# Performance work log

Measured on AMD Instinct MI355X. Metric: run time of the kernel, lower is better.

## Reference

```python
import jax, jax.numpy as jnp
import numpy as np
from math import log, sqrt

B, S, D, H, L = 16, 512, 512, 8, 6
DPH = D // H
DFF = 2048
VOCAB = 1024
MAXDEG = 64
NPC, NS = 4096, 4096


def setup_inputs() -> dict:
    rng = np.random.default_rng(0)
    raw_x = rng.integers(0, VOCAB + 1, (B, S)).astype(np.int32)
    scatter_degree = rng.integers(0, MAXDEG + 1, (B, S)).astype(np.int32)

    def uniq_triples(n, seed):
        r = np.random.default_rng(seed)
        flat = r.choice(B * S * S, n, replace=False)  # unique (b,i,j)
        b, i, j = np.unravel_index(flat, (B, S, S))
        return np.stack([b, i, j], 1).astype(np.int32)

    parentchild_indices = uniq_triples(NPC, 1)
    silbing_indices = uniq_triples(NS, 2)
    parent_child_now = np.stack([np.arange(B), rng.integers(0, S, B)], 1).astype(np.int32)
    silbing_now = np.stack([np.arange(B), rng.integers(0, S, B)], 1).astype(np.int32)

    key = jax.random.key(0)
    ks = jax.random.split(key, 16)
    sc = 0.02
    inp = {
        "raw_x": jnp.asarray(raw_x),
        "scatter_degree": jnp.asarray(scatter_degree),
        "parentchild_indices": jnp.asarray(parentchild_indices),
        "parent_child_now": jnp.asarray(parent_child_now),
        "silbing_indices": jnp.asarray(silbing_indices),
        "silbing_now": jnp.asarray(silbing_now),
        "vocab_emb": jax.random.normal(ks[0], (VOCAB + 1, D), jnp.float32) * sc,
        "degree_emb": jax.random.normal(ks[1], (MAXDEG + 1, D), jnp.float32) * sc,
        "active_rel_emb": jax.random.normal(ks[2], (2, D), jnp.float32) * sc,
        "relation_encoder": jax.random.uniform(ks[3], (3,), jnp.float32),
        "Wq": jax.random.normal(ks[4], (L, D, D), jnp.float32) * sc,
        "bq": jnp.zeros((L, D), jnp.float32),
        "Wk": jax.random.normal(ks[5], (L, D, D), jnp.float32) * sc,
        "bk": jnp.zeros((L, D), jnp.float32),
        "Wv": jax.random.normal(ks[6], (L, D, D), jnp.float32) * sc,
        "bv": jnp.zeros((L, D), jnp.float32),
        "Wo": jax.random.normal(ks[7], (L, D, D), jnp.float32) * sc,
        "bo": jnp.zeros((L, D), jnp.float32),
        "W1": jax.random.normal(ks[8], (L, DFF, D), jnp.float32) * sc,
        "b1": jnp.zeros((L, DFF), jnp.float32),
        "W2": jax.random.normal(ks[9], (L, D, DFF), jnp.float32) * sc,
        "b2": jnp.zeros((L, D), jnp.float32),
        "ln_g": jnp.ones((L, D), jnp.float32),
        "ln_b": jnp.zeros((L, D), jnp.float32),
        "logits_w": jax.random.normal(ks[10], (VOCAB, D), jnp.float32) * sc,
    }
    return inp


def _layer_norm(x, g, b):
    m = jnp.mean(x, -1, keepdims=True)
    v = jnp.mean((x - m) ** 2, -1, keepdims=True)  # biased var, eps=1e-5 (torch default)
    return (x - m) * jax.lax.rsqrt(v + 1e-5) * g + b


def _forward(raw_x, scatter_degree, parentchild_indices, parent_child_now,
             silbing_indices, silbing_now, vocab_emb, degree_emb, active_rel_emb,
             relation_encoder, Wq, bq, Wk, bk, Wv, bv, Wo, bo, W1, b1, W2, b2,
             ln_g, ln_b, logits_w):
    x = vocab_emb[raw_x]  # [B,S,D]
    # sinusoidal positional encoding
    pos = jnp.arange(S, dtype=jnp.float32)[:, None]
    div = jnp.exp(jnp.arange(0, D, 2, dtype=jnp.float32) * (-log(10000.0) / D))
    pe = jnp.zeros((S, D), x.dtype).at[:, 0::2].set(jnp.sin(pos * div)).at[:, 1::2].set(jnp.cos(pos * div))
    x = x + pe
    # structural encodings
    x = x + degree_emb[scatter_degree]
    x = x.at[parent_child_now[:, 0], parent_child_now[:, 1]].add(active_rel_emb[0])
    x = x.at[silbing_now[:, 0], silbing_now[:, 1]].add(active_rel_emb[1])

    pb, pi, pj = parentchild_indices[:, 0], parentchild_indices[:, 1], parentchild_indices[:, 2]
    sb, si, sj = silbing_indices[:, 0], silbing_indices[:, 1], silbing_indices[:, 2]
    inv_norm = 1.0 / sqrt(DPH)

    for l in range(L):
        q = (x @ Wq[l].T + bq[l]).reshape(B, S, H, DPH).transpose(0, 2, 1, 3)
        k = (x @ Wk[l].T + bk[l]).reshape(B, S, H, DPH).transpose(0, 2, 1, 3)
        v = (x @ Wv[l].T + bv[l]).reshape(B, S, H, DPH).transpose(0, 2, 1, 3)
        scores = jnp.einsum('bhqd,bhkd->bhqk', q, k) * inv_norm  # [B,H,S,S]
        # scatter-added relational bias (broadcast over all heads)
        scores = scores.at[pb, :, pi, pj].add(relation_encoder[0])
        scores = scores.at[pb, :, pj, pi].add(relation_encoder[1])
        scores = scores.at[sb, :, si, sj].add(relation_encoder[2])
        scores = scores.at[sb, :, sj, si].add(relation_encoder[2])
        attn = jax.nn.softmax(scores, axis=-1)
        o = jnp.einsum('bhqk,bhkd->bhqd', attn, v).transpose(0, 2, 1, 3).reshape(B, S, D)
        o = o @ Wo[l].T + bo[l]
        x = _layer_norm(x + o, ln_g[l], ln_b[l])
        ff = jax.nn.relu(x @ W1[l].T + b1[l]) @ W2[l].T + b2[l]
        x = _layer_norm(x + ff, ln_g[l], ln_b[l])

    return x[:, -1] @ logits_w.T  # [B, VOCAB]


def reference(raw_x, scatter_degree, parentchild_indices, parent_child_now,
              silbing_indices, silbing_now, vocab_emb, degree_emb, active_rel_emb,
              relation_encoder, Wq, bq, Wk, bk, Wv, bv, Wo, bo, W1, b1, W2, b2,
              ln_g, ln_b, logits_w):
    return _forward(raw_x, scatter_degree, parentchild_indices, parent_child_now,
                    silbing_indices, silbing_now, vocab_emb, degree_emb, active_rel_emb,
                    relation_encoder, Wq, bq, Wk, bk, Wv, bv, Wo, bo, W1, b1, W2, b2,
                    ln_g, ln_b, logits_w)
```

## Files before the change

### kernel.cpp

```cpp
#include <hip/hip_runtime.h>
#include <hip/hip_bf16.h>
#include <math.h>

#define B_ 16
#define S_ 512
#define D_ 512
#define H_ 8
#define L_ 6
#define DPH_ 64
#define DFF_ 2048
#define VOCAB_ 1024
#define NPC_ 4096
#define NS_ 4096
#define BS_ (B_ * S_)
#define LOG2E 1.4426950408889634f

typedef __attribute__((ext_vector_type(8))) short bf16x8;
typedef __attribute__((ext_vector_type(4))) float f32x4;

__device__ __forceinline__ ushort f2bf(float f) {
    __hip_bfloat16 h = __float2bfloat16(f);
    return __builtin_bit_cast(ushort, h);
}
__device__ __forceinline__ float bf2f(ushort u) {
    unsigned int v = ((unsigned int)u) << 16;
    return __builtin_bit_cast(float, v);
}

__global__ __launch_bounds__(256) void embed_kernel(
    const int* __restrict__ raw_x, const int* __restrict__ sdeg,
    const float* __restrict__ vemb, const float* __restrict__ demb,
    float* __restrict__ x)
{
    size_t idx = (size_t)blockIdx.x * 256 + threadIdx.x;
    int d = (int)(idx & (D_ - 1));
    size_t bs = idx >> 9;
    int s = (int)(bs & (S_ - 1));
    int tok = raw_x[bs];
    int dg  = sdeg[bs];
    float e = expf(-(float)(d & ~1) * (9.210340371976184f / (float)D_));
    float ang = (float)s * e;
    float pe = (d & 1) ? cosf(ang) : sinf(ang);
    x[idx] = vemb[(size_t)tok * D_ + d] + pe + demb[(size_t)dg * D_ + d];
}

__global__ void relnow_kernel(const int* __restrict__ pcn, const int* __restrict__ sbn,
                              const float* __restrict__ arel, float* __restrict__ x)
{
    int b = blockIdx.x;
    int t = threadIdx.x;
    int b1 = pcn[b * 2 + 0], p1 = pcn[b * 2 + 1];
    x[((size_t)(b1 * S_ + p1)) * D_ + t] += arel[t];
    int b2 = sbn[b * 2 + 0], p2 = sbn[b * 2 + 1];
    x[((size_t)(b2 * S_ + p2)) * D_ + t] += arel[D_ + t];
}

__global__ void bias_scatter_kernel(const int* __restrict__ pc, const int* __restrict__ sb,
                                    const float* __restrict__ renc, float* __restrict__ bias)
{
    int t = blockIdx.x * 256 + threadIdx.x;
    float r0 = renc[0], r1 = renc[1], r2 = renc[2];
    if (t < NPC_) {
        int b = pc[t * 3 + 0], i = pc[t * 3 + 1], j = pc[t * 3 + 2];
        atomicAdd(&bias[((size_t)b * S_ + i) * S_ + j], r0);
        atomicAdd(&bias[((size_t)b * S_ + j) * S_ + i], r1);
    } else if (t < NPC_ + NS_) {
        int u = t - NPC_;
        int b = sb[u * 3 + 0], i = sb[u * 3 + 1], j = sb[u * 3 + 2];
        atomicAdd(&bias[((size_t)b * S_ + i) * S_ + j], r2);
        atomicAdd(&bias[((size_t)b * S_ + j) * S_ + i], r2);
    }
}

__global__ __launch_bounds__(256) void bias_cast_kernel(const float* __restrict__ src,
                                                        ushort* __restrict__ dst)
{
    int i = blockIdx.x * 256 + threadIdx.x;
    float4 v = ((const float4*)src)[i];
    ushort4 o;
    o.x = f2bf(v.x * LOG2E); o.y = f2bf(v.y * LOG2E);
    o.z = f2bf(v.z * LOG2E); o.w = f2bf(v.w * LOG2E);
    ((ushort4*)dst)[i] = o;
}

__global__ __launch_bounds__(256) void cast4_kernel(const float* __restrict__ src,
                                                    ushort* __restrict__ dst, int n4)
{
    int i = blockIdx.x * 256 + threadIdx.x;
    if (i >= n4) return;
    float4 v = ((const float4*)src)[i];
    ushort4 o;
    o.x = f2bf(v.x); o.y = f2bf(v.y); o.z = f2bf(v.z); o.w = f2bf(v.w);
    ((ushort4*)dst)[i] = o;
}

__global__ __launch_bounds__(256) void pack_qkv_kernel(
    const float* __restrict__ Wq, const float* __restrict__ Wk, const float* __restrict__ Wv,
    ushort* __restrict__ dst)
{
    int idx = blockIdx.x * 256 + threadIdx.x;
    int c = idx & 511;
    int rl = idx >> 9;
    int r = rl % 1536, l = rl / 1536;
    float v;
    if (r < 512)       v = Wq[((size_t)l * 512 + r) * 512 + c];
    else if (r < 1024) v = Wk[((size_t)l * 512 + (r - 512)) * 512 + c];
    else               v = Wv[((size_t)l * 512 + (r - 1024)) * 512 + c];
    dst[idx] = f2bf(v);
}

__global__ void pack_bqkv_kernel(const float* __restrict__ bq, const float* __restrict__ bk,
                                 const float* __restrict__ bv, float* __restrict__ dst)
{
    int idx = blockIdx.x * 256 + threadIdx.x;
    if (idx >= L_ * 1536) return;
    int r = idx % 1536, l = idx / 1536;
    float v;
    if (r < 512)       v = bq[l * 512 + r];
    else if (r < 1024) v = bk[l * 512 + r - 512];
    else               v = bv[l * 512 + r - 1024];
    dst[idx] = v;
}

#define GL2LDS(g, l) __builtin_amdgcn_global_load_lds( \
    (const __attribute__((address_space(1))) void*)(g), \
    (__attribute__((address_space(3))) void*)(l), 16, 0, 0)

__global__ __launch_bounds__(256) void gemm_bf16(
    const ushort* __restrict__ A, const ushort* __restrict__ W,
    const float* __restrict__ bias, ushort* __restrict__ Cb,
    int K, int M, int mode)
{
    __shared__ ushort As[128 * 32];
    __shared__ ushort Bs[128 * 32];

    const int t  = threadIdx.x;
    const int wv = t >> 6;
    const int ln = t & 63;
    const int wm = wv >> 1, wn = wv & 1;
    const int row0 = blockIdx.y * 128;
    const int col0 = blockIdx.x * 128;
    const int lr = ln >> 2;
    const int lk = (ln & 3) * 8;

    f32x4 acc[4][4] = {};

    for (int k0 = 0; k0 < K; k0 += 32) {
        #pragma unroll
        for (int i = 0; i < 2; i++) {
            int r = i * 64 + wv * 16;
            const ushort* ga = A + (size_t)(row0 + r + lr) * K + k0 + lk;
            const ushort* gb = W + (size_t)(col0 + r + lr) * K + k0 + lk;
            GL2LDS(ga, &As[r * 32]);
            GL2LDS(gb, &Bs[r * 32]);
        }
        __syncthreads();

        bf16x8 af[4], bf[4];
        #pragma unroll
        for (int mi = 0; mi < 4; mi++)
            af[mi] = *(const bf16x8*)&As[(wm * 64 + mi * 16 + (ln & 15)) * 32 + (ln >> 4) * 8];
        #pragma unroll
        for (int ni = 0; ni < 4; ni++)
            bf[ni] = *(const bf16x8*)&Bs[(wn * 64 + ni * 16 + (ln & 15)) * 32 + (ln >> 4) * 8];
        #pragma unroll
        for (int mi = 0; mi < 4; mi++)
            #pragma unroll
            for (int ni = 0; ni < 4; ni++)
                acc[mi][ni] = __builtin_amdgcn_mfma_f32_16x16x32_bf16(af[mi], bf[ni], acc[mi][ni], 0, 0, 0);
        __syncthreads();
    }

    const int lq = ln >> 4, lc = ln & 15;
    #pragma unroll
    for (int mi = 0; mi < 4; mi++) {
        #pragma unroll
        for (int ni = 0; ni < 4; ni++) {
            int gcol = col0 + wn * 64 + ni * 16 + lc;
            float bb = bias[gcol];
            #pragma unroll
            for (int rr = 0; rr < 4; rr++) {
                int grow = row0 + wm * 64 + mi * 16 + lq * 4 + rr;
                float val = acc[mi][ni][rr] + bb;
                if (mode == 1) val = fmaxf(val, 0.f);
                Cb[(size_t)grow * M + gcol] = f2bf(val);
            }
        }
    }
}

__global__ __launch_bounds__(256) void gemm_bf16_sk(
    const ushort* __restrict__ A, const ushort* __restrict__ W,
    ushort* __restrict__ Cp, int K, int M)
{
    __shared__ ushort As[128 * 32];
    __shared__ ushort Bs[128 * 32];

    const int t  = threadIdx.x;
    const int wv = t >> 6;
    const int ln = t & 63;
    const int wm = wv >> 1, wn = wv & 1;
    const int row0 = blockIdx.y * 128;
    const int col0 = blockIdx.x * 128;
    const int z    = blockIdx.z;
    const int Kh   = K >> 1;
    const int lr = ln >> 2;
    const int lk = (ln & 3) * 8;

    const ushort* Az = A + (size_t)z * Kh;
    const ushort* Wz = W + (size_t)z * Kh;

    f32x4 acc[4][4] = {};

    for (int k0 = 0; k0 < Kh; k0 += 32) {
        #pragma unroll
        for (int i = 0; i < 2; i++) {
            int r = i * 64 + wv * 16;
            const ushort* ga = Az + (size_t)(row0 + r + lr) * K + k0 + lk;
            const ushort* gb = Wz + (size_t)(col0 + r + lr) * K + k0 + lk;
            GL2LDS(ga, &As[r * 32]);
            GL2LDS(gb, &Bs[r * 32]);
        }
        __syncthreads();

        bf16x8 af[4], bf[4];
        #pragma unroll
        for (int mi = 0; mi < 4; mi++)
            af[mi] = *(const bf16x8*)&As[(wm * 64 + mi * 16 + (ln & 15)) * 32 + (ln >> 4) * 8];
        #pragma unroll
        for (int ni = 0; ni < 4; ni++)
            bf[ni] = *(const bf16x8*)&Bs[(wn * 64 + ni * 16 + (ln & 15)) * 32 + (ln >> 4) * 8];
        #pragma unroll
        for (int mi = 0; mi < 4; mi++)
            #pragma unroll
            for (int ni = 0; ni < 4; ni++)
                acc[mi][ni] = __builtin_amdgcn_mfma_f32_16x16x32_bf16(af[mi], bf[ni], acc[mi][ni], 0, 0, 0);
        __syncthreads();
    }

    ushort* Cz = Cp + (size_t)z * BS_ * M;
    const int lq = ln >> 4, lc = ln & 15;
    #pragma unroll
    for (int mi = 0; mi < 4; mi++)
        #pragma unroll
        for (int ni = 0; ni < 4; ni++) {
            int gcol = col0 + wn * 64 + ni * 16 + lc;
            #pragma unroll
            for (int rr = 0; rr < 4; rr++) {
                int grow = row0 + wm * 64 + mi * 16 + lq * 4 + rr;
                Cz[(size_t)grow * M + gcol] = f2bf(acc[mi][ni][rr]);
            }
        }
}

#define PSTR 72

__device__ __forceinline__ int vswz(int d, int j) {
    int g = ((j >> 3) ^ (d & 7) ^ ((d >> 3) & 7)) & 7;
    return d * 64 + g * 8 + (j & 7);
}

__global__ __launch_bounds__(256) void attn_kernel(
    const ushort* __restrict__ qkv, const ushort* __restrict__ biasb,
    ushort* __restrict__ ao)
{
    const int qt = blockIdx.x, h = blockIdx.y, b = blockIdx.z;
    const int t  = threadIdx.x;
    const int wq = t >> 6;
    const int ln = t & 63;
    const int lq = ln >> 4;
    const int lc = ln & 15;
    const int r  = t >> 2;
    const int cg = t & 3;

    __shared__ ushort Qs[64 * PSTR];
    __shared__ ushort Ks[64 * PSTR];
    __shared__ ushort Ps[64 * PSTR];
    __shared__ ushort Vts[64 * 64];

    const int i0 = qt * 64;

    {
        const ushort* qsrc = qkv + (size_t)(b * S_ + i0 + r) * 1536 + h * 64 + cg * 16;
        *(uint4*)&Qs[r * PSTR + cg * 16]     = ((const uint4*)qsrc)[0];
        *(uint4*)&Qs[r * PSTR + cg * 16 + 8] = ((const uint4*)qsrc)[1];
    }
    bf16x8 aq0 = *(const bf16x8*)&Qs[(wq * 16 + lc) * PSTR + lq * 8];
    bf16x8 aq1 = *(const bf16x8*)&Qs[(wq * 16 + lc) * PSTR + 32 + lq * 8];

    f32x4 of[4] = {};
    float l_lane[4] = {};
    const float QSC = 0.125f * LOG2E;

    for (int j0 = 0; j0 < S_; j0 += 64) {
        __syncthreads();
        {
            const ushort* ksrc = qkv + (size_t)(b * S_ + j0 + r) * 1536 + 512 + h * 64 + cg * 16;
            *(uint4*)&Ks[r * PSTR + cg * 16]     = ((const uint4*)ksrc)[0];
            *(uint4*)&Ks[r * PSTR + cg * 16 + 8] = ((const uint4*)ksrc)[1];
            const ushort* vsrc = ksrc + 512;
            ushort vv[16];
            *(uint4*)&vv[0] = ((const uint4*)vsrc)[0];
            *(uint4*)&vv[8] = ((const uint4*)vsrc)[1];
            #pragma unroll
            for (int dd = 0; dd < 16; dd++)
                Vts[vswz(cg * 16 + dd, r)] = vv[dd];
        }
        __syncthreads();

        f32x4 sf[4] = {};
        #pragma unroll
        for (int ni = 0; ni < 4; ni++) {
            bf16x8 bk0 = *(const bf16x8*)&Ks[(ni * 16 + lc) * PSTR + lq * 8];
            bf16x8 bk1 = *(const bf16x8*)&Ks[(ni * 16 + lc) * PSTR + 32 + lq * 8];
            sf[ni] = __builtin_amdgcn_mfma_f32_16x16x32_bf16(aq0, bk0, sf[ni], 0, 0, 0);
            sf[ni] = __builtin_amdgcn_mfma_f32_16x16x32_bf16(aq1, bk1, sf[ni], 0, 0, 0);
        }

        const ushort* bbase = biasb + (size_t)(b * S_ + i0 + wq * 16 + lq * 4) * S_ + j0;
        #pragma unroll
        for (int ni = 0; ni < 4; ni++)
            #pragma unroll
            for (int rr = 0; rr < 4; rr++) {
                float bv = bf2f(bbase[(size_t)rr * S_ + ni * 16 + lc]);
                float p = __builtin_amdgcn_exp2f(fmaf(sf[ni][rr], QSC, bv));
                l_lane[rr] += p;
                Ps[(wq * 16 + lq * 4 + rr) * PSTR + ni * 16 + lc] = f2bf(p);
            }

        bf16x8 ap0 = *(const bf16x8*)&Ps[(wq * 16 + lc) * PSTR + lq * 8];
        bf16x8 ap1 = *(const bf16x8*)&Ps[(wq * 16 + lc) * PSTR + 32 + lq * 8];
        #pragma unroll
        for (int ni = 0; ni < 4; ni++) {
            bf16x8 bv0 = *(const bf16x8*)&Vts[vswz(ni * 16 + lc, lq * 8)];
            bf16x8 bv1 = *(const bf16x8*)&Vts[vswz(ni * 16 + lc, 32 + lq * 8)];
            of[ni] = __builtin_amdgcn_mfma_f32_16x16x32_bf16(ap0, bv0, of[ni], 0, 0, 0);
            of[ni] = __builtin_amdgcn_mfma_f32_16x16x32_bf16(ap1, bv1, of[ni], 0, 0, 0);
        }
    }

    float inv[4];
    #pragma unroll
    for (int rr = 0; rr < 4; rr++) {
        float s = l_lane[rr];
        s += __shfl_xor(s, 1);
        s += __shfl_xor(s, 2);
        s += __shfl_xor(s, 4);
        s += __shfl_xor(s, 8);
        inv[rr] = 1.f / s;
    }
    #pragma unroll
    for (int ni = 0; ni < 4; ni++)
        #pragma unroll
        for (int rr = 0; rr < 4; rr++) {
            int row = i0 + wq * 16 + lq * 4 + rr;
            ao[(size_t)(b * S_ + row) * D_ + h * 64 + ni * 16 + lc] = f2bf(of[ni][rr] * inv[rr]);
        }
}

__device__ __forceinline__ float block_sum(float v, float* red) {
    #pragma unroll
    for (int off = 32; off > 0; off >>= 1) v += __shfl_down(v, off);
    int t = threadIdx.x;
    if ((t & 63) == 0) red[t >> 6] = v;
    __syncthreads();
    float r = red[0] + red[1] + red[2] + red[3];
    __syncthreads();
    return r;
}

__global__ __launch_bounds__(256) void add_ln_kernel(
    float* __restrict__ x, const ushort* __restrict__ p0, const ushort* __restrict__ p1,
    const float* __restrict__ bvec,
    const float* __restrict__ g, const float* __restrict__ bta,
    ushort* __restrict__ xb)
{
    __shared__ float red[4];
    const int row = blockIdx.x;
    const int t = threadIdx.x;
    const size_t base = (size_t)row * D_;
    float v0 = x[base + t]       + bf2f(p0[base + t])       + bf2f(p1[base + t])       + bvec[t];
    float v1 = x[base + t + 256] + bf2f(p0[base + t + 256]) + bf2f(p1[base + t + 256]) + bvec[t + 256];
    float mean = block_sum(v0 + v1, red) * (1.f / (float)D_);
    float d0 = v0 - mean, d1 = v1 - mean;
    float var = block_sum(d0 * d0 + d1 * d1, red) * (1.f / (float)D_);
    float inv = rsqrtf(var + 1e-5f);
    float o0 = d0 * inv * g[t] + bta[t];
    float o1 = d1 * inv * g[t + 256] + bta[t + 256];
    x[base + t] = o0;
    x[base + t + 256] = o1;
    xb[base + t] = f2bf(o0);
    xb[base + t + 256] = f2bf(o1);
}

__global__ __launch_bounds__(256) void logits_kernel(
    const float* __restrict__ x, const float* __restrict__ lw, float* __restrict__ out)
{
    __shared__ float xs[D_];
    const int b = blockIdx.x;
    const int vchunk = blockIdx.y;
    const int t = threadIdx.x;
    const float* xrow = x + ((size_t)(b * S_ + (S_ - 1)) * D_);
    xs[t] = xrow[t];
    xs[t + 256] = xrow[t + 256];
    __syncthreads();
    for (int vv = vchunk * 128 + t; vv < vchunk * 128 + 128; vv += 256) {
        const float* wr = lw + (size_t)vv * D_;
        float acc = 0.f;
        #pragma unroll 8
        for (int d = 0; d < D_; d += 4) {
            float4 w4 = *(const float4*)&wr[d];
            acc += xs[d] * w4.x + xs[d + 1] * w4.y + xs[d + 2] * w4.z + xs[d + 3] * w4.w;
        }
        out[(size_t)b * VOCAB_ + vv] = acc;
    }
}

extern "C" void kernel_launch(void* const* d_in, const int* in_sizes, int n_in,
                              void* d_out, int out_size, void* d_ws, size_t ws_size,
                              hipStream_t stream)
{
    const int* raw_x = (const int*)d_in[0];
    const int* sdeg  = (const int*)d_in[1];
    const int* pci   = (const int*)d_in[2];
    const int* pcn   = (const int*)d_in[3];
    const int* sbi   = (const int*)d_in[4];
    const int* sbn   = (const int*)d_in[5];
    const float* vemb = (const float*)d_in[6];
    const float* demb = (const float*)d_in[7];
    const float* arel = (const float*)d_in[8];
    const float* renc = (const float*)d_in[9];
    const float* Wq = (const float*)d_in[10];
    const float* bq = (const float*)d_in[11];
    const float* Wk = (const float*)d_in[12];
    const float* bk = (const float*)d_in[13];
    const float* Wv = (const float*)d_in[14];
    const float* bv = (const float*)d_in[15];
    const float* Wo = (const float*)d_in[16];
    const float* bo = (const float*)d_in[17];
    const float* W1 = (const float*)d_in[18];
    const float* b1 = (const float*)d_in[19];
    const float* W2 = (const float*)d_in[20];
    const float* b2 = (const float*)d_in[21];
    const float* lng = (const float*)d_in[22];
    const float* lnb = (const float*)d_in[23];
    const float* lw  = (const float*)d_in[24];
    float* out = (float*)d_out;

    float* wsf = (float*)d_ws;
    const size_t X = (size_t)BS_ * D_;
    float*  x    = wsf;
    ushort* xb   = (ushort*)(wsf + X);
    ushort* qkvb = (ushort*)(wsf + (X * 3) / 2);
    ushort* ao   = (ushort*)(wsf + 3 * X);
    ushort* h1   = (ushort*)(wsf + (X * 7) / 2);
    ushort* part = (ushort*)(wsf + (X * 11) / 2);
    float*  bias = wsf + (X * 13) / 2;
    ushort* biasb= (ushort*)(wsf + (X * 15) / 2);
    ushort* wb   = (ushort*)(wsf + 8 * X);
    ushort* wqkv_b = wb;
    ushort* wo_b   = wb + 4718592;
    ushort* w1_b   = wb + 6291456;
    ushort* w2_b   = wb + 12582912;
    float*  bqkv   = wsf + 8 * X + 9437184;

    embed_kernel<<<(B_ * S_ * D_) / 256, 256, 0, stream>>>(raw_x, sdeg, vemb, demb, x);
    relnow_kernel<<<B_, D_, 0, stream>>>(pcn, sbn, arel, x);
    cast4_kernel<<<(int)(X / 4 / 256), 256, 0, stream>>>(x, xb, (int)(X / 4));

    hipMemsetAsync(bias, 0, (size_t)B_ * S_ * S_ * sizeof(float), stream);
    bias_scatter_kernel<<<(NPC_ + NS_ + 255) / 256, 256, 0, stream>>>(pci, sbi, renc, bias);
    bias_cast_kernel<<<(B_ * S_ * S_ / 4) / 256, 256, 0, stream>>>(bias, biasb);

    pack_qkv_kernel<<<(L_ * 1536 * 512) / 256, 256, 0, stream>>>(Wq, Wk, Wv, wqkv_b);
    pack_bqkv_kernel<<<(L_ * 1536 + 255) / 256, 256, 0, stream>>>(bq, bk, bv, bqkv);
    cast4_kernel<<<(L_ * 512 * 512) / 4 / 256, 256, 0, stream>>>(Wo, wo_b, L_ * 512 * 512 / 4);
    cast4_kernel<<<(L_ * 2048 * 512) / 4 / 256, 256, 0, stream>>>(W1, w1_b, L_ * 2048 * 512 / 4);
    cast4_kernel<<<(L_ * 512 * 2048) / 4 / 256, 256, 0, stream>>>(W2, w2_b, L_ * 512 * 2048 / 4);

    dim3 blk(256);
    for (int l = 0; l < L_; l++) {
        gemm_bf16<<<dim3(1536 / 128, BS_ / 128), blk, 0, stream>>>(
            xb, wqkv_b + (size_t)l * 1536 * 512, bqkv + l * 1536, qkvb, 512, 1536, 2);

        attn_kernel<<<dim3(S_ / 64, H_, B_), blk, 0, stream>>>(qkvb, biasb, ao);

        gemm_bf16_sk<<<dim3(512 / 128, BS_ / 128, 2), blk, 0, stream>>>(
            ao, wo_b + (size_t)l * 512 * 512, part, 512, 512);
        add_ln_kernel<<<BS_, blk, 0, stream>>>(x, part, part + (size_t)BS_ * 512,
                                               bo + l * 512, lng + l * D_, lnb + l * D_, xb);

        gemm_bf16<<<dim3(2048 / 128, BS_ / 128), blk, 0, stream>>>(
            xb, w1_b + (size_t)l * 2048 * 512, b1 + l * 2048, h1, 512, 2048, 1);
        gemm_bf16_sk<<<dim3(512 / 128, BS_ / 128, 2), blk, 0, stream>>>(
            h1, w2_b + (size_t)l * 512 * 2048, part, 2048, 512);
        add_ln_kernel<<<BS_, blk, 0, stream>>>(x, part, part + (size_t)BS_ * 512,
                                               b2 + l * 512, lng + l * D_, lnb + l * D_, xb);
    }

    logits_kernel<<<dim3(B_, 8), blk, 0, stream>>>(x, lw, out);
}
```

Measured before the change: 1.165 ms.

## Deepen GEMM K-step to 64 and replace split-K projections with 128x64 tiles

The main GEMM now loads two 32-wide K slabs per iteration, halving the number of barrier pairs per K loop. The two split-K output GEMMs (Wo and W2) are replaced by a non-split 128x64-tile GEMM that writes fp32 results directly. add_ln then reads a single fp32 buffer instead of summing two bf16 partials. This removes the partial write/read traffic and the bf16 rounding of the partials, at the cost of larger fp32 output writes and more LDS per block, which may reduce occupancy.

```diff
diff --git a/kernel.cpp b/kernel.cpp
--- a/kernel.cpp
+++ b/kernel.cpp
@@ -131,13 +131,16 @@
     const float* __restrict__ bias, ushort* __restrict__ Cb,
     int K, int M, int mode)
 {
-    __shared__ ushort As[128 * 32];
-    __shared__ ushort Bs[128 * 32];
+    __shared__ ushort As0[128 * 32];
+    __shared__ ushort As1[128 * 32];
+    __shared__ ushort Bs0[128 * 32];
+    __shared__ ushort Bs1[128 * 32];
 
     const int t  = threadIdx.x;
     const int wv = t >> 6;
     const int ln = t & 63;
     const int wm = wv >> 1, wn = wv & 1;
+    const int lq = ln >> 4, lc = ln & 15;
     const int row0 = blockIdx.y * 128;
     const int col0 = blockIdx.x * 128;
     const int lr = ln >> 2;
@@ -145,24 +148,38 @@
 
     f32x4 acc[4][4] = {};
 
-    for (int k0 = 0; k0 < K; k0 += 32) {
+    for (int k0 = 0; k0 < K; k0 += 64) {
         #pragma unroll
         for (int i = 0; i < 2; i++) {
             int r = i * 64 + wv * 16;
             const ushort* ga = A + (size_t)(row0 + r + lr) * K + k0 + lk;
             const ushort* gb = W + (size_t)(col0 + r + lr) * K + k0 + lk;
-            GL2LDS(ga, &As[r * 32]);
-            GL2LDS(gb, &Bs[r * 32]);
+            GL2LDS(ga,      &As0[r * 32]);
+            GL2LDS(gb,      &Bs0[r * 32]);
+            GL2LDS(ga + 32, &As1[r * 32]);
+            GL2LDS(gb + 32, &Bs1[r * 32]);
         }
         __syncthreads();
 
         bf16x8 af[4], bf[4];
         #pragma unroll
         for (int mi = 0; mi < 4; mi++)
-            af[mi] = *(const bf16x8*)&As[(wm * 64 + mi * 16 + (ln & 15)) * 32 + (ln >> 4) * 8];
+            af[mi] = *(const bf16x8*)&As0[(wm * 64 + mi * 16 + lc) * 32 + lq * 8];
         #pragma unroll
         for (int ni = 0; ni < 4; ni++)
-            bf[ni] = *(const bf16x8*)&Bs[(wn * 64 + ni * 16 + (ln & 15)) * 32 + (ln >> 4) * 8];
+            bf[ni] = *(const bf16x8*)&Bs0[(wn * 64 + ni * 16 + lc) * 32 + lq * 8];
+        #pragma unroll
+        for (int mi = 0; mi < 4; mi++)
+            #pragma unroll
+            for (int ni = 0; ni < 4; ni++)
+                acc[mi][ni] = __builtin_amdgcn_mfma_f32_16x16x32_bf16(af[mi], bf[ni], acc[mi][ni], 0, 0, 0);
+
+        #pragma unroll
+        for (int mi = 0; mi < 4; mi++)
+            af[mi] = *(const bf16x8*)&As1[(wm * 64 + mi * 16 + lc) * 32 + lq * 8];
+        #pragma unroll
+        for (int ni = 0; ni < 4; ni++)
+            bf[ni] = *(const bf16x8*)&Bs1[(wn * 64 + ni * 16 + lc) * 32 + lq * 8];
         #pragma unroll
         for (int mi = 0; mi < 4; mi++)
             #pragma unroll
@@ -171,7 +188,6 @@
         __syncthreads();
     }
 
-    const int lq = ln >> 4, lc = ln & 15;
     #pragma unroll
     for (int mi = 0; mi < 4; mi++) {
         #pragma unroll
@@ -189,66 +205,79 @@
     }
 }
 
-__global__ __launch_bounds__(256) void gemm_bf16_sk(
+__global__ __launch_bounds__(256) void gemm64(
     const ushort* __restrict__ A, const ushort* __restrict__ W,
-    ushort* __restrict__ Cp, int K, int M)
-{
-    __shared__ ushort As[128 * 32];
-    __shared__ ushort Bs[128 * 32];
+    float* __restrict__ C, int K, int M)
+{
+    __shared__ ushort As0[128 * 32];
+    __shared__ ushort As1[128 * 32];
+    __shared__ ushort Bs0[64 * 32];
+    __shared__ ushort Bs1[64 * 32];
 
     const int t  = threadIdx.x;
     const int wv = t >> 6;
     const int ln = t & 63;
     const int wm = wv >> 1, wn = wv & 1;
+    const int lq = ln >> 4, lc = ln & 15;
     const int row0 = blockIdx.y * 128;
-    const int col0 = blockIdx.x * 128;
-    const int z    = blockIdx.z;
-    const int Kh   = K >> 1;
+    const int col0 = blockIdx.x * 64;
     const int lr = ln >> 2;
     const int lk = (ln & 3) * 8;
 
-    const ushort* Az = A + (size_t)z * Kh;
-    const ushort* Wz = W + (size_t)z * Kh;
-
-    f32x4 acc[4][4] = {};
-
-    for (int k0 = 0; k0 < Kh; k0 += 32) {
+    f32x4 acc[4][2] = {};
+
+    for (int k0 = 0; k0 < K; k0 += 64) {
         #pragma unroll
         for (int i = 0; i < 2; i++) {
             int r = i * 64 + wv * 16;
-            const ushort* ga = Az + (size_t)(row0 + r + lr) * K + k0 + lk;
-            const ushort* gb = Wz + (size_t)(col0 + r + lr) * K + k0 + lk;
-            GL2LDS(ga, &As[r * 32]);
-            GL2LDS(gb, &Bs[r * 32]);
+            const ushort* ga = A + (size_t)(row0 + r + lr) * K + k0 + lk;
+            GL2LDS(ga,      &As0[r * 32]);
+            GL2LDS(ga + 32, &As1[r * 32]);
+        }
+        {
+            int rb = wv * 16;
+            const ushort* gb = W + (size_t)(col0 + rb + lr) * K + k0 + lk;
+            GL2LDS(gb,      &Bs0[rb * 32]);
+            GL2LDS(gb + 32, &Bs1[rb * 32]);
         }
         __syncthreads();
 
-        bf16x8 af[4], bf[4];
-        #pragma unroll
-        for (int mi = 0; mi < 4; mi++)
-            af[mi] = *(const bf16x8*)&As[(wm * 64 + mi * 16 + (ln & 15)) * 32 + (ln >> 4) * 8];
-        #pragma unroll
-        for (int ni = 0; ni < 4; ni++)
-            bf[ni] = *(const bf16x8*)&Bs[(wn * 64 + ni * 16 + (ln & 15)) * 32 + (ln >> 4) * 8];
-        #pragma unroll
-        for (int mi = 0; mi < 4; mi++)
-            #pragma unroll
-            for (int ni = 0; ni < 4; ni++)
+        bf16x8 af[4], bf[2];
+        #pragma unroll
+        for (int mi = 0; mi < 4; mi++)
+            af[mi] = *(const bf16x8*)&As0[(wm * 64 + mi * 16 + lc) * 32 + lq * 8];
+        #pragma unroll
+        for (int ni = 0; ni < 2; ni++)
+            bf[ni] = *(const bf16x8*)&Bs0[(wn * 32 + ni * 16 + lc) * 32 + lq * 8];
+        #pragma unroll
+        for (int mi = 0; mi < 4; mi++)
+            #pragma unroll
+            for (int ni = 0; ni < 2; ni++)
+                acc[mi][ni] = __builtin_amdgcn_mfma_f32_16x16x32_bf16(af[mi], bf[ni], acc[mi][ni], 0, 0, 0);
+
+        #pragma unroll
+        for (int mi = 0; mi < 4; mi++)
+            af[mi] = *(const bf16x8*)&As1[(wm * 64 + mi * 16 + lc) * 32 + lq * 8];
+        #pragma unroll
+        for (int ni = 0; ni < 2; ni++)
+            bf[ni] = *(const bf16x8*)&Bs1[(wn * 32 + ni * 16 + lc) * 32 + lq * 8];
+        #pragma unroll
+        for (int mi = 0; mi < 4; mi++)
+            #pragma unroll
+            for (int ni = 0; ni < 2; ni++)
                 acc[mi][ni] = __builtin_amdgcn_mfma_f32_16x16x32_bf16(af[mi], bf[ni], acc[mi][ni], 0, 0, 0);
         __syncthreads();
     }
 
-    ushort* Cz = Cp + (size_t)z * BS_ * M;
-    const int lq = ln >> 4, lc = ln & 15;
     #pragma unroll
     for (int mi = 0; mi < 4; mi++)
         #pragma unroll
-        for (int ni = 0; ni < 4; ni++) {
-            int gcol = col0 + wn * 64 + ni * 16 + lc;
+        for (int ni = 0; ni < 2; ni++) {
+            int gcol = col0 + wn * 32 + ni * 16 + lc;
             #pragma unroll
             for (int rr = 0; rr < 4; rr++) {
                 int grow = row0 + wm * 64 + mi * 16 + lq * 4 + rr;
-                Cz[(size_t)grow * M + gcol] = f2bf(acc[mi][ni][rr]);
+                C[(size_t)grow * M + gcol] = acc[mi][ni][rr];
             }
         }
 }
@@ -370,7 +399,7 @@
 }
 
 __global__ __launch_bounds__(256) void add_ln_kernel(
-    float* __restrict__ x, const ushort* __restrict__ p0, const ushort* __restrict__ p1,
+    float* __restrict__ x, const float* __restrict__ p,
     const float* __restrict__ bvec,
     const float* __restrict__ g, const float* __restrict__ bta,
     ushort* __restrict__ xb)
@@ -379,8 +408,8 @@
     const int row = blockIdx.x;
     const int t = threadIdx.x;
     const size_t base = (size_t)row * D_;
-    float v0 = x[base + t]       + bf2f(p0[base + t])       + bf2f(p1[base + t])       + bvec[t];
-    float v1 = x[base + t + 256] + bf2f(p0[base + t + 256]) + bf2f(p1[base + t + 256]) + bvec[t + 256];
+    float v0 = x[base + t]       + p[base + t]       + bvec[t];
+    float v1 = x[base + t + 256] + p[base + t + 256] + bvec[t + 256];
     float mean = block_sum(v0 + v1, red) * (1.f / (float)D_);
     float d0 = v0 - mean, d1 = v1 - mean;
     float var = block_sum(d0 * d0 + d1 * d1, red) * (1.f / (float)D_);
@@ -454,7 +483,7 @@
     ushort* qkvb = (ushort*)(wsf + (X * 3) / 2);
     ushort* ao   = (ushort*)(wsf + 3 * X);
     ushort* h1   = (ushort*)(wsf + (X * 7) / 2);
-    ushort* part = (ushort*)(wsf + (X * 11) / 2);
+    float*  proj = wsf + (X * 11) / 2;
     float*  bias = wsf + (X * 13) / 2;
     ushort* biasb= (ushort*)(wsf + (X * 15) / 2);
     ushort* wb   = (ushort*)(wsf + 8 * X);
@@ -485,17 +514,17 @@
 
         attn_kernel<<<dim3(S_ / 64, H_, B_), blk, 0, stream>>>(qkvb, biasb, ao);
 
-        gemm_bf16_sk<<<dim3(512 / 128, BS_ / 128, 2), blk, 0, stream>>>(
-            ao, wo_b + (size_t)l * 512 * 512, part, 512, 512);
-        add_ln_kernel<<<BS_, blk, 0, stream>>>(x, part, part + (size_t)BS_ * 512,
-                                               bo + l * 512, lng + l * D_, lnb + l * D_, xb);
+        gemm64<<<dim3(512 / 64, BS_ / 128), blk, 0, stream>>>(
+            ao, wo_b + (size_t)l * 512 * 512, proj, 512, 512);
+        add_ln_kernel<<<BS_, blk, 0, stream>>>(x, proj, bo + l * 512,
+                                               lng + l * D_, lnb + l * D_, xb);
 
         gemm_bf16<<<dim3(2048 / 128, BS_ / 128), blk, 0, stream>>>(
             xb, w1_b + (size_t)l * 2048 * 512, b1 + l * 2048, h1, 512, 2048, 1);
-        gemm_bf16_sk<<<dim3(512 / 128, BS_ / 128, 2), blk, 0, stream>>>(
-            h1, w2_b + (size_t)l * 512 * 2048, part, 2048, 512);
-        add_ln_kernel<<<BS_, blk, 0, stream>>>(x, part, part + (size_t)BS_ * 512,
-                                               b2 + l * 512, lng + l * D_, lnb + l * D_, xb);
+        gemm64<<<dim3(512 / 64, BS_ / 128), blk, 0, stream>>>(
+            h1, w2_b + (size_t)l * 512 * 2048, proj, 2048, 512);
+        add_ln_kernel<<<BS_, blk, 0, stream>>>(x, proj, b2 + l * 512,
+                                               lng + l * D_, lnb + l * D_, xb);
     }
 
     logits_kernel<<<dim3(B_, 8), blk, 0, stream>>>(x, lw, out);
```

New measurement: 1.220 ms. 1.05x slower.
